# Performance work log

Hardware: AMD Instinct MI355X
Metric: run time of the kernel (lower is better)

## Reference

```python
import jax, jax.numpy as jnp
import numpy as np

N_NODES = 500_000
D_IN = 256
D_ATT = 128
NUM_GRAPHS = 4096


def setup_inputs() -> dict:
    key = jax.random.key(0)
    k_x, k_b, k_w1, k_b1, k_w2, k_b2 = jax.random.split(key, 6)
    x = jax.random.normal(k_x, (N_NODES, D_IN), dtype=jnp.float32)
    batch = jnp.sort(jax.random.randint(k_b, (N_NODES,), 0, NUM_GRAPHS, dtype=jnp.int64))
    # attention_net params: Linear(D_IN, D_ATT) -> tanh -> Linear(D_ATT, 1)
    s1 = 1.0 / np.sqrt(D_IN)
    s2 = 1.0 / np.sqrt(D_ATT)
    W1 = jax.random.uniform(k_w1, (D_IN, D_ATT), minval=-s1, maxval=s1, dtype=jnp.float32)
    b1 = jax.random.uniform(k_b1, (D_ATT,), minval=-s1, maxval=s1, dtype=jnp.float32)
    W2 = jax.random.uniform(k_w2, (D_ATT, 1), minval=-s2, maxval=s2, dtype=jnp.float32)
    b2 = jax.random.uniform(k_b2, (1,), minval=-s2, maxval=s2, dtype=jnp.float32)
    return {"x": x, "batch": batch, "num_graphs": NUM_GRAPHS,
            "W1": W1, "b1": b1, "W2": W2, "b2": b2}


def reference(x, batch, num_graphs, W1, b1, W2, b2):
    # attention_weights = Linear -> tanh -> Linear  (dropout is identity in eval)
    h = jnp.tanh(x @ W1 + b1)              # [N, D_ATT]
    attn = h @ W2 + b2                      # [N, 1]
    weighted_x = x * attn                   # [N, D_IN]
    # global_add_pool: segment-sum over graph ids
    return jax.ops.segment_sum(weighted_x, batch, num_segments=num_graphs)  # [B, D_IN]
```

## Files before the change

kernel.cpp:

```cpp
#include <hip/hip_runtime.h>
#include <hip/hip_bf16.h>

#define NN     500000
#define DIN    256
#define DATT   128
#define NG     4096
#define MT     32
#define NT32   15625
#define NBLOCKS 512
#define TPB    31

typedef __attribute__((ext_vector_type(8))) short short8;
typedef __attribute__((ext_vector_type(4))) float f32x4;

__device__ __forceinline__ unsigned int pack2bf(float a, float b) {
    unsigned int ua = __float_as_uint(a) + 0x8000u;
    unsigned int ub = __float_as_uint(b) + 0x8000u;
    return __builtin_amdgcn_perm(ub, ua, 0x07060302);
}

__device__ __forceinline__ float tanh_fast(float v) {
    float e = __expf(2.f * v);
    return 1.f - 2.f * __builtin_amdgcn_rcpf(e + 1.f);
}

__device__ __forceinline__ void lds_barrier() {
    asm volatile("s_waitcnt lgkmcnt(0)" ::: "memory");
    __builtin_amdgcn_s_barrier();
    asm volatile("" ::: "memory");
}

__global__ void prep_w1t(const float* __restrict__ W1, unsigned short* __restrict__ W1t) {
    int c = blockIdx.x;
    int k = threadIdx.x;
    unsigned int u = __float_as_uint(W1[k * DATT + c]) + 0x8000u;
    W1t[c * DIN + k] = (unsigned short)(u >> 16);
}

__global__ __launch_bounds__(512, 4)
void attnpool_kernel(const float* __restrict__ x,
                     const int* __restrict__ batch,
                     const unsigned short* __restrict__ W1t,
                     const float* __restrict__ b1,
                     const float* __restrict__ W2,
                     const float* __restrict__ b2,
                     float* __restrict__ out)
{
    __shared__ unsigned short xb[2][MT * DIN];
    __shared__ float part[8][MT];

    const int t0 = blockIdx.x * TPB;
    if (t0 >= NT32) return;
    const int tEnd = (t0 + TPB < NT32) ? t0 + TPB : NT32;

    const int tid = threadIdx.x;
    const int w   = tid >> 6;
    const int l   = tid & 63;
    const int lr  = l & 15;
    const int lg  = l >> 4;

    short8 afr[8];
    {
        const unsigned short* A0 = W1t + (16 * w + lr) * DIN;
        #pragma unroll
        for (int kc = 0; kc < 8; ++kc)
            afr[kc] = *reinterpret_cast<const short8*>(A0 + 32 * kc + 8 * lg);
    }
    float4 b1v, w2v;
    {
        int c0 = 16 * w + 4 * lg;
        b1v = *reinterpret_cast<const float4*>(&b1[c0]);
        w2v = *reinterpret_cast<const float4*>(&W2[c0]);
    }
    const float b2s = b2[0];

    const float4* xg = (const float4*)x;
    float4 pf[4];
    {
        int base = t0 * (MT * 64);
        #pragma unroll
        for (int i = 0; i < 4; ++i) pf[i] = xg[base + tid + i * 512];
    }

    float accum = 0.f;
    int gcur = -1;
    int cur = 0;
    const int half = tid >> 8;
    const int d    = tid & 255;

    for (int t = t0; t < tEnd; ++t) {
        unsigned short* X = xb[cur];
        #pragma unroll
        for (int i = 0; i < 4; ++i) {
            int j = tid + i * 512;
            int r = j >> 6, c4 = j & 63;
            int byte = r * 512 + ((c4 * 8) ^ ((r & 7) << 4));
            *reinterpret_cast<uint2*>(reinterpret_cast<char*>(X) + byte) =
                make_uint2(pack2bf(pf[i].x, pf[i].y), pack2bf(pf[i].z, pf[i].w));
        }
        int bvt = -1;
        if (l < 32) {
            int g = batch[t * MT + l];
            bvt = ((unsigned)g < NG) ? g : -1;
        }
        lds_barrier();

        if (t + 1 < tEnd) {
            int base = (t + 1) * (MT * 64);
            #pragma unroll
            for (int i = 0; i < 4; ++i) pf[i] = xg[base + tid + i * 512];
        }

        f32x4 acc[2];
        acc[0] = (f32x4){0.f, 0.f, 0.f, 0.f};
        acc[1] = (f32x4){0.f, 0.f, 0.f, 0.f};

        #pragma unroll
        for (int kc = 0; kc < 8; ++kc) {
            int ko = 32 * kc + 8 * lg;
            short8 bfr[2];
            #pragma unroll
            for (int ct = 0; ct < 2; ++ct) {
                int row = 16 * ct + lr;
                int byte = row * 512 + ((ko * 2) ^ ((row & 7) << 4));
                bfr[ct] = *reinterpret_cast<const short8*>(reinterpret_cast<const char*>(X) + byte);
            }
            acc[0] = __builtin_amdgcn_mfma_f32_16x16x32_bf16(afr[kc], bfr[0], acc[0], 0, 0, 0);
            acc[1] = __builtin_amdgcn_mfma_f32_16x16x32_bf16(afr[kc], bfr[1], acc[1], 0, 0, 0);
        }

        #pragma unroll
        for (int ct = 0; ct < 2; ++ct) {
            float p = tanh_fast(acc[ct][0] + b1v.x) * w2v.x
                    + tanh_fast(acc[ct][1] + b1v.y) * w2v.y
                    + tanh_fast(acc[ct][2] + b1v.z) * w2v.z
                    + tanh_fast(acc[ct][3] + b1v.w) * w2v.w;
            p += __shfl_xor(p, 16, 64);
            p += __shfl_xor(p, 32, 64);
            if (lg == 0) part[w][16 * ct + lr] = p;
        }
        lds_barrier();

        const int nd = l & 31;
        float va = b2s + part[0][nd] + part[1][nd] + part[2][nd] + part[3][nd]
                       + part[4][nd] + part[5][nd] + part[6][nd] + part[7][nd];

        #pragma unroll
        for (int n = 0; n < 16; ++n) {
            int node = 16 * half + n;
            int   g = __builtin_amdgcn_readlane(bvt, node);
            float a = __int_as_float(__builtin_amdgcn_readlane(__float_as_int(va), node));
            if (g != gcur) {
                if (gcur >= 0) atomicAdd(&out[gcur * DIN + d], accum);
                accum = 0.f;
                gcur = g;
            }
            int byte = node * 512 + ((d * 2) ^ ((node & 7) << 4));
            float xv = __uint_as_float(
                (unsigned int)(*reinterpret_cast<const unsigned short*>(
                    reinterpret_cast<const char*>(X) + byte)) << 16);
            accum = fmaf(a, xv, accum);
        }
        cur ^= 1;
    }
    if (gcur >= 0) atomicAdd(&out[gcur * DIN + d], accum);
}

extern "C" void kernel_launch(void* const* d_in, const int* in_sizes, int n_in,
                              void* d_out, int out_size, void* d_ws, size_t ws_size,
                              hipStream_t stream) {
    const float* x     = (const float*)d_in[0];
    const int*   batch = (const int*)d_in[1];
    const float* W1 = (const float*)d_in[3];
    const float* b1 = (const float*)d_in[4];
    const float* W2 = (const float*)d_in[5];
    const float* b2 = (const float*)d_in[6];
    float* out = (float*)d_out;
    unsigned short* W1t = (unsigned short*)d_ws;

    hipMemsetAsync(out, 0, (size_t)NG * DIN * sizeof(float), stream);
    prep_w1t<<<DATT, DIN, 0, stream>>>(W1, W1t);
    attnpool_kernel<<<NBLOCKS, 512, 0, stream>>>(x, batch, W1t, b1, W2, b2, out);
}
```

Baseline: 136.6 us.

## Pool from fp32 prefetch registers instead of bf16 LDS tile

The weighted segment-sum now uses the fp32 x values already held in registers from the prefetch, instead of re-reading bf16 values from the shared tile. Each thread accumulates four contiguous columns for the node rows it loaded, so the pooling no longer reads LDS and uses full precision. In exchange it holds a second set of prefetch registers, which can hurt occupancy. Each thread now walks every eighth node, so runs of one graph split into more segment flushes, each issuing four atomics.

```diff
diff --git a/kernel.cpp b/kernel.cpp
--- a/kernel.cpp
+++ b/kernel.cpp
@@ -58,6 +58,7 @@
     const int l   = tid & 63;
     const int lr  = l & 15;
     const int lg  = l >> 4;
+    const int c4  = tid & 63;
 
     short8 afr[8];
     {
@@ -82,19 +83,17 @@
         for (int i = 0; i < 4; ++i) pf[i] = xg[base + tid + i * 512];
     }
 
-    float accum = 0.f;
+    float4 acc4 = make_float4(0.f, 0.f, 0.f, 0.f);
     int gcur = -1;
     int cur = 0;
-    const int half = tid >> 8;
-    const int d    = tid & 255;
 
     for (int t = t0; t < tEnd; ++t) {
         unsigned short* X = xb[cur];
         #pragma unroll
         for (int i = 0; i < 4; ++i) {
             int j = tid + i * 512;
-            int r = j >> 6, c4 = j & 63;
-            int byte = r * 512 + ((c4 * 8) ^ ((r & 7) << 4));
+            int r = j >> 6, cc = j & 63;
+            int byte = r * 512 + ((cc * 8) ^ ((r & 7) << 4));
             *reinterpret_cast<uint2*>(reinterpret_cast<char*>(X) + byte) =
                 make_uint2(pack2bf(pf[i].x, pf[i].y), pack2bf(pf[i].z, pf[i].w));
         }
@@ -105,10 +104,14 @@
         }
         lds_barrier();
 
+        float4 pfn[4];
         if (t + 1 < tEnd) {
             int base = (t + 1) * (MT * 64);
             #pragma unroll
-            for (int i = 0; i < 4; ++i) pf[i] = xg[base + tid + i * 512];
+            for (int i = 0; i < 4; ++i) pfn[i] = xg[base + tid + i * 512];
+        } else {
+            #pragma unroll
+            for (int i = 0; i < 4; ++i) pfn[i] = pf[i];
         }
 
         f32x4 acc[2];
@@ -146,24 +149,34 @@
                        + part[4][nd] + part[5][nd] + part[6][nd] + part[7][nd];
 
         #pragma unroll
-        for (int n = 0; n < 16; ++n) {
-            int node = 16 * half + n;
+        for (int i = 0; i < 4; ++i) {
+            int node = w + 8 * i;
             int   g = __builtin_amdgcn_readlane(bvt, node);
             float a = __int_as_float(__builtin_amdgcn_readlane(__float_as_int(va), node));
             if (g != gcur) {
-                if (gcur >= 0) atomicAdd(&out[gcur * DIN + d], accum);
-                accum = 0.f;
+                if (gcur >= 0) {
+                    float* o = &out[gcur * DIN + 4 * c4];
+                    atomicAdd(o + 0, acc4.x); atomicAdd(o + 1, acc4.y);
+                    atomicAdd(o + 2, acc4.z); atomicAdd(o + 3, acc4.w);
+                }
+                acc4 = make_float4(0.f, 0.f, 0.f, 0.f);
                 gcur = g;
             }
-            int byte = node * 512 + ((d * 2) ^ ((node & 7) << 4));
-            float xv = __uint_as_float(
-                (unsigned int)(*reinterpret_cast<const unsigned short*>(
-                    reinterpret_cast<const char*>(X) + byte)) << 16);
-            accum = fmaf(a, xv, accum);
+            acc4.x = fmaf(a, pf[i].x, acc4.x);
+            acc4.y = fmaf(a, pf[i].y, acc4.y);
+            acc4.z = fmaf(a, pf[i].z, acc4.z);
+            acc4.w = fmaf(a, pf[i].w, acc4.w);
         }
+
+        #pragma unroll
+        for (int i = 0; i < 4; ++i) pf[i] = pfn[i];
         cur ^= 1;
     }
-    if (gcur >= 0) atomicAdd(&out[gcur * DIN + d], accum);
+    if (gcur >= 0) {
+        float* o = &out[gcur * DIN + 4 * c4];
+        atomicAdd(o + 0, acc4.x); atomicAdd(o + 1, acc4.y);
+        atomicAdd(o + 2, acc4.z); atomicAdd(o + 3, acc4.w);
+    }
 }
 
 extern "C" void kernel_launch(void* const* d_in, const int* in_sizes, int n_in,
```

Result: slower. 227.0 us (+66.2%).

## Double node tile to 64 rows and balance tiles evenly across blocks

Applied to the files above, without the earlier changes.

Raises the per-iteration node tile from 32 to 64 rows, so each wave issues four MFMAs per k-chunk against the register-resident W1 fragment and barriers are amortized over twice the nodes. Tiles are now split across the 512 blocks by proportional ranges instead of a fixed count per block, which removes the imbalance where the last blocks got fewer tiles. Bounds checks handle the final partial tile. LDS use doubles to 64 KB and each thread holds twice the prefetch registers, which may reduce occupancy.

```diff
diff --git a/kernel.cpp b/kernel.cpp
--- a/kernel.cpp
+++ b/kernel.cpp
@@ -5,10 +5,9 @@
 #define DIN    256
 #define DATT   128
 #define NG     4096
-#define MT     32
-#define NT32   15625
+#define MT     64
+#define NT64   7813
 #define NBLOCKS 512
-#define TPB    31
 
 typedef __attribute__((ext_vector_type(8))) short short8;
 typedef __attribute__((ext_vector_type(4))) float f32x4;
@@ -49,9 +48,10 @@
     __shared__ unsigned short xb[2][MT * DIN];
     __shared__ float part[8][MT];
 
-    const int t0 = blockIdx.x * TPB;
-    if (t0 >= NT32) return;
-    const int tEnd = (t0 + TPB < NT32) ? t0 + TPB : NT32;
+    const int bidx = blockIdx.x;
+    const int t0   = (int)(((long long)bidx * NT64) / NBLOCKS);
+    const int tEnd = (int)(((long long)(bidx + 1) * NT64) / NBLOCKS);
+    if (t0 >= tEnd) return;
 
     const int tid = threadIdx.x;
     const int w   = tid >> 6;
@@ -75,11 +75,12 @@
     const float b2s = b2[0];
 
     const float4* xg = (const float4*)x;
-    float4 pf[4];
-    {
-        int base = t0 * (MT * 64);
-        #pragma unroll
-        for (int i = 0; i < 4; ++i) pf[i] = xg[base + tid + i * 512];
+    float4 pf[8];
+    #pragma unroll
+    for (int i = 0; i < 8; ++i) {
+        int j = tid + i * 512;
+        long long n = (long long)t0 * MT + (j >> 6);
+        pf[i] = (n < NN) ? xg[t0 * 4096 + j] : make_float4(0.f, 0.f, 0.f, 0.f);
     }
 
     float accum = 0.f;
@@ -91,46 +92,53 @@
     for (int t = t0; t < tEnd; ++t) {
         unsigned short* X = xb[cur];
         #pragma unroll
-        for (int i = 0; i < 4; ++i) {
+        for (int i = 0; i < 8; ++i) {
             int j = tid + i * 512;
-            int r = j >> 6, c4 = j & 63;
-            int byte = r * 512 + ((c4 * 8) ^ ((r & 7) << 4));
+            int r = j >> 6, cc = j & 63;
+            int byte = r * 512 + ((cc * 8) ^ ((r & 7) << 4));
             *reinterpret_cast<uint2*>(reinterpret_cast<char*>(X) + byte) =
                 make_uint2(pack2bf(pf[i].x, pf[i].y), pack2bf(pf[i].z, pf[i].w));
         }
         int bvt = -1;
-        if (l < 32) {
-            int g = batch[t * MT + l];
-            bvt = ((unsigned)g < NG) ? g : -1;
+        {
+            long long n = (long long)t * MT + l;
+            if (n < NN) {
+                int g = batch[n];
+                bvt = ((unsigned)g < NG) ? g : -1;
+            }
         }
         lds_barrier();
 
         if (t + 1 < tEnd) {
-            int base = (t + 1) * (MT * 64);
             #pragma unroll
-            for (int i = 0; i < 4; ++i) pf[i] = xg[base + tid + i * 512];
+            for (int i = 0; i < 8; ++i) {
+                int j = tid + i * 512;
+                long long n = (long long)(t + 1) * MT + (j >> 6);
+                pf[i] = (n < NN) ? xg[(t + 1) * 4096 + j] : make_float4(0.f, 0.f, 0.f, 0.f);
+            }
         }
 
-        f32x4 acc[2];
-        acc[0] = (f32x4){0.f, 0.f, 0.f, 0.f};
-        acc[1] = (f32x4){0.f, 0.f, 0.f, 0.f};
+        f32x4 acc[4];
+        #pragma unroll
+        for (int ct = 0; ct < 4; ++ct) acc[ct] = (f32x4){0.f, 0.f, 0.f, 0.f};
 
         #pragma unroll
         for (int kc = 0; kc < 8; ++kc) {
             int ko = 32 * kc + 8 * lg;
-            short8 bfr[2];
+            short8 bfr[4];
             #pragma unroll
-            for (int ct = 0; ct < 2; ++ct) {
+            for (int ct = 0; ct < 4; ++ct) {
                 int row = 16 * ct + lr;
                 int byte = row * 512 + ((ko * 2) ^ ((row & 7) << 4));
                 bfr[ct] = *reinterpret_cast<const short8*>(reinterpret_cast<const char*>(X) + byte);
             }
-            acc[0] = __builtin_amdgcn_mfma_f32_16x16x32_bf16(afr[kc], bfr[0], acc[0], 0, 0, 0);
-            acc[1] = __builtin_amdgcn_mfma_f32_16x16x32_bf16(afr[kc], bfr[1], acc[1], 0, 0, 0);
+            #pragma unroll
+            for (int ct = 0; ct < 4; ++ct)
+                acc[ct] = __builtin_amdgcn_mfma_f32_16x16x32_bf16(afr[kc], bfr[ct], acc[ct], 0, 0, 0);
         }
 
         #pragma unroll
-        for (int ct = 0; ct < 2; ++ct) {
+        for (int ct = 0; ct < 4; ++ct) {
             float p = tanh_fast(acc[ct][0] + b1v.x) * w2v.x
                     + tanh_fast(acc[ct][1] + b1v.y) * w2v.y
                     + tanh_fast(acc[ct][2] + b1v.z) * w2v.z
@@ -141,13 +149,12 @@
         }
         lds_barrier();
 
-        const int nd = l & 31;
-        float va = b2s + part[0][nd] + part[1][nd] + part[2][nd] + part[3][nd]
-                       + part[4][nd] + part[5][nd] + part[6][nd] + part[7][nd];
+        float va = b2s + part[0][l] + part[1][l] + part[2][l] + part[3][l]
+                       + part[4][l] + part[5][l] + part[6][l] + part[7][l];
 
         #pragma unroll
-        for (int n = 0; n < 16; ++n) {
-            int node = 16 * half + n;
+        for (int n = 0; n < 32; ++n) {
+            int node = 32 * half + n;
             int   g = __builtin_amdgcn_readlane(bvt, node);
             float a = __int_as_float(__builtin_amdgcn_readlane(__float_as_int(va), node));
             if (g != gcur) {
```

After: 377.5 us. 176% more time.
